# Kernel optimization log

Hardware: AMD Instinct MI355X
Metric: run time of the kernel (lower is better)

Reference implementation:

```python
import jax, jax.numpy as jnp
import numpy as np

# ROI Align config (module attributes in the original torch wrapper)
SPATIAL_SCALE = 0.25
POOLED_H = 7
POOLED_W = 7
SAMPLE_NUM = 2
ROI_END_MODE = 1  # Ascend: end coord gets +roi_end_mode before scaling


def setup_inputs() -> dict:
    key = jax.random.key(0)
    k_feat, k_b, k_xy, k_wh = jax.random.split(key, 4)
    B, C, H, W = 2, 256, 200, 200
    N = 1000
    feat = jax.random.normal(k_feat, (B, C, H, W), dtype=jnp.float32)
    img_h, img_w = H / SPATIAL_SCALE, W / SPATIAL_SCALE
    bidx = jax.random.randint(k_b, (N,), 0, B).astype(jnp.float32)
    xy = jax.random.uniform(k_xy, (N, 2), dtype=jnp.float32)
    wh = jax.random.uniform(k_wh, (N, 2), dtype=jnp.float32)
    x1 = xy[:, 0] * (img_w - 64.0)
    y1 = xy[:, 1] * (img_h - 64.0)
    x2 = x1 + 8.0 + wh[:, 0] * 200.0
    y2 = y1 + 8.0 + wh[:, 1] * 200.0
    rois = jnp.stack([bidx, x1, y1, x2, y2], axis=1)  # [N,5]
    return {"input": feat, "rois": rois}


def _axis_coords(start, bin_size, pooled, sn):
    # sample coord for grid index g: start + bin_size*(g+0.5)/sn, g in [0, pooled*sn)
    g = jnp.arange(pooled * sn, dtype=jnp.float32)
    return start[:, None] + bin_size[:, None] * (g[None, :] + 0.5) / sn  # [N, pooled*sn]


def _bilinear_1d(c, size):
    # returns (low_idx, high_idx, w_low, w_high, valid) for coordinate array c
    valid = (c >= -1.0) & (c <= size)
    cc = jnp.clip(c, 0.0, size - 1.0)
    lo = jnp.floor(cc).astype(jnp.int32)
    lo = jnp.clip(lo, 0, size - 1)
    hi = jnp.clip(lo + 1, 0, size - 1)
    frac = cc - lo.astype(jnp.float32)
    return lo, hi, 1.0 - frac, frac, valid


def roi_align(feat, rois):
    B, C, H, W = feat.shape
    N = rois.shape[0]
    bidx = rois[:, 0].astype(jnp.int32)
    off = float(ROI_END_MODE)
    x1 = rois[:, 1] * SPATIAL_SCALE
    y1 = rois[:, 2] * SPATIAL_SCALE
    x2 = (rois[:, 3] + off) * SPATIAL_SCALE
    y2 = (rois[:, 4] + off) * SPATIAL_SCALE
    roi_w = jnp.maximum(x2 - x1, 1.0)
    roi_h = jnp.maximum(y2 - y1, 1.0)
    bin_h = roi_h / POOLED_H
    bin_w = roi_w / POOLED_W

    ys = _axis_coords(y1, bin_h, POOLED_H, SAMPLE_NUM)  # [N, GY]
    xs = _axis_coords(x1, bin_w, POOLED_W, SAMPLE_NUM)  # [N, GX]
    yl, yh, wyl, wyh, vy = _bilinear_1d(ys, H)
    xl, xh, wxl, wxh, vx = _bilinear_1d(xs, W)

    b = bidx[:, None, None]

    def gather(yi, xi):
        # advanced indexing -> [N, GY, GX, C]
        return feat[b, :, yi[:, :, None], xi[:, None, :]]

    val = (wyl[:, :, None, None] * wxl[:, None, :, None] * gather(yl, xl)
           + wyl[:, :, None, None] * wxh[:, None, :, None] * gather(yl, xh)
           + wyh[:, :, None, None] * wxl[:, None, :, None] * gather(yh, xl)
           + wyh[:, :, None, None] * wxh[:, None, :, None] * gather(yh, xh))
    mask = (vy[:, :, None] & vx[:, None, :]).astype(val.dtype)[..., None]
    val = val * mask  # [N, GY, GX, C]

    # average pool over the SAMPLE_NUM x SAMPLE_NUM grid inside each bin
    val = val.reshape(N, POOLED_H, SAMPLE_NUM, POOLED_W, SAMPLE_NUM, C)
    out = val.mean(axis=(2, 4))  # [N, PH, PW, C]
    return jnp.transpose(out, (0, 3, 1, 2))  # [N, C, PH, PW]


def reference(input, rois):
    return roi_align(input, rois)
```

## Files before the change

### kernel.cpp

```cpp
#include <hip/hip_runtime.h>
#include <hip/hip_bf16.h>


constexpr int C_TOT  = 256;
constexpr int H_FEAT = 200;
constexpr int W_FEAT = 200;
constexpr int HW     = H_FEAT * W_FEAT;
constexpr int S_TOT  = 49;
constexpr size_t FEATT_BYTES = (size_t)2 * HW * C_TOT * sizeof(unsigned short);
constexpr int NXCD = 8;
constexpr int NBUCKET = 32;

__global__ __launch_bounds__(1024) void roi_bin_kernel(
    const float* __restrict__ rois, int* __restrict__ perm, int N)
{
    __shared__ int hist[NBUCKET];
    __shared__ int base[NBUCKET];
    __shared__ int cnt[NBUCKET];
    int t = threadIdx.x;

    if (t < NBUCKET) { hist[t] = 0; cnt[t] = 0; }
    __syncthreads();

    int bucket = -1;
    if (t < N) {
        const float* r = rois + (size_t)t * 5;
        int   b  = (int)r[0];
        float cx = (r[1] + r[3]) * 0.5f * 0.25f;
        float cy = (r[2] + r[4]) * 0.5f * 0.25f;
        int qx = min(max((int)(cx * (4.0f / 200.0f)), 0), 3);
        int qy = min(max((int)(cy * (4.0f / 200.0f)), 0), 3);
        bucket = ((b & 1) << 4) | (qy << 2) | qx;
        atomicAdd(&hist[bucket], 1);
    }
    __syncthreads();

    if (t == 0) {
        int acc = 0;
        for (int i = 0; i < NBUCKET; ++i) { base[i] = acc; acc += hist[i]; }
    }
    __syncthreads();

    if (t < N) {
        int pos = base[bucket] + atomicAdd(&cnt[bucket], 1);
        perm[pos] = t;
    }
}

__global__ __launch_bounds__(256) void nchw_to_nhwc_bf16_kernel(
    const float* __restrict__ feat,
    unsigned short* __restrict__ featT)
{
    __shared__ float tile[32][33];
    int tx = threadIdx.x;
    int ty = threadIdx.y;
    int s0 = blockIdx.x * 32;
    int c0 = blockIdx.y * 32;
    int b  = blockIdx.z;

    const float* src = feat + ((size_t)b * C_TOT) * HW;
    #pragma unroll
    for (int i = 0; i < 4; ++i) {
        int r = ty + i * 8;
        tile[r][tx] = src[(size_t)(c0 + r) * HW + (s0 + tx)];
    }
    __syncthreads();
    unsigned short* dst = featT + ((size_t)b * HW) * C_TOT;
    #pragma unroll
    for (int i = 0; i < 4; ++i) {
        int r = ty + i * 8;
        float x = tile[tx][r];
        unsigned int u = __float_as_uint(x);
        unsigned int rb = (u + 0x7fffu + ((u >> 16) & 1u)) >> 16;
        dst[(size_t)(s0 + r) * C_TOT + (c0 + tx)] = (unsigned short)rb;
    }
}

__global__ __launch_bounds__(512) void roi_align_nhwc_kernel(
    const unsigned short* __restrict__ featT,
    const float* __restrict__ rois,
    const int* __restrict__ perm,
    float* __restrict__ out,
    int N, int use_perm)
{
    __shared__ alignas(16) float tile[C_TOT * S_TOT];

    int n;
    if (use_perm) {
        int chunk = (N + NXCD - 1) / NXCD;
        int rank  = (blockIdx.x & (NXCD - 1)) * chunk + (blockIdx.x >> 3);
        if (rank >= N) rank = blockIdx.x;
        n = perm[rank];
    } else {
        n = blockIdx.x;
    }

    int tid  = threadIdx.x;
    int wave = tid >> 6;
    int lane = tid & 63;

    const float* r = rois + (size_t)n * 5;
    int   b  = (int)r[0];
    float x1 = r[1] * 0.25f;
    float y1 = r[2] * 0.25f;
    float x2 = (r[3] + 1.0f) * 0.25f;
    float y2 = (r[4] + 1.0f) * 0.25f;
    float bin_w = fmaxf(x2 - x1, 1.0f) * (1.0f / 7.0f);
    float bin_h = fmaxf(y2 - y1, 1.0f) * (1.0f / 7.0f);

    const unsigned short* fbase =
        featT + (size_t)b * HW * C_TOT + (size_t)lane * 4;

    for (int s = wave; s < S_TOT; s += 8) {
        int ph = s / 7;
        int pw = s - ph * 7;

        int   yoff[2][2];
        int   xoff[2][2];
        float wy[2][2], wx[2][2];
        #pragma unroll
        for (int i = 0; i < 2; ++i) {
            float gy  = (float)(2 * ph + i);
            float cy  = y1 + bin_h * ((gy + 0.5f) * 0.5f);
            bool  vy  = (cy >= -1.0f) && (cy <= (float)H_FEAT);
            float ccy = fminf(fmaxf(cy, 0.0f), (float)(H_FEAT - 1));
            int   ylo = (int)ccy;
            int   yhi = min(ylo + 1, H_FEAT - 1);
            float fy  = ccy - (float)ylo;
            yoff[i][0] = ylo * W_FEAT;
            yoff[i][1] = yhi * W_FEAT;
            wy[i][0] = vy ? (1.0f - fy) * 0.5f : 0.0f;
            wy[i][1] = vy ? fy * 0.5f          : 0.0f;

            float gx  = (float)(2 * pw + i);
            float cx  = x1 + bin_w * ((gx + 0.5f) * 0.5f);
            bool  vx  = (cx >= -1.0f) && (cx <= (float)W_FEAT);
            float ccx = fminf(fmaxf(cx, 0.0f), (float)(W_FEAT - 1));
            int   xlo = (int)ccx;
            int   xhi = min(xlo + 1, W_FEAT - 1);
            float fx  = ccx - (float)xlo;
            xoff[i][0] = xlo;
            xoff[i][1] = xhi;
            wx[i][0] = vx ? (1.0f - fx) * 0.5f : 0.0f;
            wx[i][1] = vx ? fx * 0.5f          : 0.0f;
        }

        float4 acc = make_float4(0.f, 0.f, 0.f, 0.f);
        #pragma unroll
        for (int iy = 0; iy < 2; ++iy)
        #pragma unroll
        for (int jy = 0; jy < 2; ++jy)
        #pragma unroll
        for (int ix = 0; ix < 2; ++ix)
        #pragma unroll
        for (int jx = 0; jx < 2; ++jx) {
            float w = wy[iy][jy] * wx[ix][jx];
            const ushort4 v = *reinterpret_cast<const ushort4*>(
                fbase + (size_t)(yoff[iy][jy] + xoff[ix][jx]) * C_TOT);
            float f0 = __uint_as_float((unsigned int)v.x << 16);
            float f1 = __uint_as_float((unsigned int)v.y << 16);
            float f2 = __uint_as_float((unsigned int)v.z << 16);
            float f3 = __uint_as_float((unsigned int)v.w << 16);
            acc.x = fmaf(w, f0, acc.x);
            acc.y = fmaf(w, f1, acc.y);
            acc.z = fmaf(w, f2, acc.z);
            acc.w = fmaf(w, f3, acc.w);
        }

        int c = lane * 4;
        tile[(c + 0) * S_TOT + s] = acc.x;
        tile[(c + 1) * S_TOT + s] = acc.y;
        tile[(c + 2) * S_TOT + s] = acc.z;
        tile[(c + 3) * S_TOT + s] = acc.w;
    }
    __syncthreads();

    const float4* t4 = reinterpret_cast<const float4*>(tile);
    float4* o4 = reinterpret_cast<float4*>(out + (size_t)n * (C_TOT * S_TOT));
    constexpr int Q = C_TOT * S_TOT / 4;
    for (int q = tid; q < Q; q += 512)
        o4[q] = t4[q];
}

constexpr int CPT = 4;
constexpr int CG  = C_TOT / CPT;

__global__ __launch_bounds__(256) void roi_align_direct_kernel(
    const float* __restrict__ feat,
    const float* __restrict__ rois,
    float* __restrict__ out,
    int N)
{
    int t = blockIdx.x * 256 + threadIdx.x;
    int total = N * CG * S_TOT;
    if (t >= total) return;

    int s   = t % S_TOT;
    int rem = t / S_TOT;
    int c0  = rem % CG;
    int n   = rem / CG;
    int ph  = s / 7;
    int pw  = s - ph * 7;

    const float* r = rois + (size_t)n * 5;
    int   b  = (int)r[0];
    float x1 = r[1] * 0.25f;
    float y1 = r[2] * 0.25f;
    float x2 = (r[3] + 1.0f) * 0.25f;
    float y2 = (r[4] + 1.0f) * 0.25f;
    float bin_w = fmaxf(x2 - x1, 1.0f) * (1.0f / 7.0f);
    float bin_h = fmaxf(y2 - y1, 1.0f) * (1.0f / 7.0f);

    int   roff[2][2], coff[2][2];
    float wy[2][2], wx[2][2];
    #pragma unroll
    for (int i = 0; i < 2; ++i) {
        float gy  = (float)(2 * ph + i);
        float cy  = y1 + bin_h * ((gy + 0.5f) * 0.5f);
        bool  vy  = (cy >= -1.0f) && (cy <= (float)H_FEAT);
        float ccy = fminf(fmaxf(cy, 0.0f), (float)(H_FEAT - 1));
        int   ylo = (int)ccy;
        int   yhi = min(ylo + 1, H_FEAT - 1);
        float fy  = ccy - (float)ylo;
        roff[i][0] = ylo * W_FEAT;
        roff[i][1] = yhi * W_FEAT;
        wy[i][0] = vy ? (1.0f - fy) : 0.0f;
        wy[i][1] = vy ? fy          : 0.0f;

        float gx  = (float)(2 * pw + i);
        float cx  = x1 + bin_w * ((gx + 0.5f) * 0.5f);
        bool  vx  = (cx >= -1.0f) && (cx <= (float)W_FEAT);
        float ccx = fminf(fmaxf(cx, 0.0f), (float)(W_FEAT - 1));
        int   xlo = (int)ccx;
        int   xhi = min(xlo + 1, W_FEAT - 1);
        float fx  = ccx - (float)xlo;
        coff[i][0] = xlo;
        coff[i][1] = xhi;
        wx[i][0] = vx ? (1.0f - fx) : 0.0f;
        wx[i][1] = vx ? fx          : 0.0f;
    }

    float w16[16];
    int   o16[16];
    #pragma unroll
    for (int iy = 0; iy < 2; ++iy)
    #pragma unroll
    for (int ix = 0; ix < 2; ++ix)
    #pragma unroll
    for (int jy = 0; jy < 2; ++jy)
    #pragma unroll
    for (int jx = 0; jx < 2; ++jx) {
        int idx = ((iy * 2 + ix) * 2 + jy) * 2 + jx;
        w16[idx] = wy[iy][jy] * wx[ix][jx];
        o16[idx] = roff[iy][jy] + coff[ix][jx];
    }

    size_t base  = ((size_t)b * C_TOT + c0) * HW;
    size_t obase = (size_t)n * (C_TOT * S_TOT) + (size_t)c0 * S_TOT + s;

    #pragma unroll
    for (int k = 0; k < CPT; ++k) {
        const float* f = feat + base + (size_t)k * CG * HW;
        float acc = 0.0f;
        #pragma unroll
        for (int j = 0; j < 16; ++j)
            acc = fmaf(w16[j], f[o16[j]], acc);
        out[obase + (size_t)k * (CG * S_TOT)] = acc * 0.25f;
    }
}

extern "C" void kernel_launch(void* const* d_in, const int* in_sizes, int n_in,
                              void* d_out, int out_size, void* d_ws, size_t ws_size,
                              hipStream_t stream) {
    const float* feat = (const float*)d_in[0];
    const float* rois = (const float*)d_in[1];
    float* out = (float*)d_out;
    int N = in_sizes[1] / 5;

    size_t need = FEATT_BYTES + 4096;
    if (ws_size >= need) {
        unsigned short* featT = (unsigned short*)d_ws;
        int* perm = (int*)((char*)d_ws + FEATT_BYTES);
        int use_perm = (N <= 1024) ? 1 : 0;
        if (use_perm)
            roi_bin_kernel<<<1, 1024, 0, stream>>>(rois, perm, N);
        dim3 tgrid(HW / 32, C_TOT / 32, 2);
        dim3 tblk(32, 8);
        nchw_to_nhwc_bf16_kernel<<<tgrid, tblk, 0, stream>>>(feat, featT);
        roi_align_nhwc_kernel<<<N, 512, 0, stream>>>(featT, rois, perm, out, N, use_perm);
    } else {
        int total  = N * CG * S_TOT;
        int blocks = (total + 255) / 256;
        roi_align_direct_kernel<<<blocks, 256, 0, stream>>>(feat, rois, out, N);
    }
}
```

Measured before the change: 61.12 us.

## Use 16-byte bf16 loads split across half-waves with XOR-swizzled LDS tile

Each half-wave now handles one of the two horizontal neighbor pixels, and each lane loads 8 bf16 channels with one 16-byte load instead of 4 channels with 8-byte loads. The two halves are summed with a cross-lane shuffle. The shared tile uses an XOR swizzle on channel index to spread LDS bank conflicts, and the output copy undoes the swizzle. This halves the number of global load instructions but adds shuffles, per-element index math in the copy-out, and idle lanes during tile writes.

```diff
diff --git a/kernel.cpp b/kernel.cpp
--- a/kernel.cpp
+++ b/kernel.cpp
@@ -98,6 +98,8 @@
     int tid  = threadIdx.x;
     int wave = tid >> 6;
     int lane = tid & 63;
+    int half = lane >> 5;
+    int li   = lane & 31;
 
     const float* r = rois + (size_t)n * 5;
     int   b  = (int)r[0];
@@ -108,8 +110,8 @@
     float bin_w = fmaxf(x2 - x1, 1.0f) * (1.0f / 7.0f);
     float bin_h = fmaxf(y2 - y1, 1.0f) * (1.0f / 7.0f);
 
-    const unsigned short* fbase =
-        featT + (size_t)b * HW * C_TOT + (size_t)lane * 4;
+    const unsigned short* fb = featT + (size_t)b * HW * C_TOT + li * 8;
+    int xorsw = (li >> 2) & 7;
 
     for (int s = wave; s < S_TOT; s += 8) {
         int ph = s / 7;
@@ -145,41 +147,66 @@
             wx[i][1] = vx ? fx * 0.5f          : 0.0f;
         }
 
-        float4 acc = make_float4(0.f, 0.f, 0.f, 0.f);
+        float acc[8];
+        #pragma unroll
+        for (int j = 0; j < 8; ++j) acc[j] = 0.0f;
+
         #pragma unroll
         for (int iy = 0; iy < 2; ++iy)
         #pragma unroll
         for (int jy = 0; jy < 2; ++jy)
         #pragma unroll
-        for (int ix = 0; ix < 2; ++ix)
-        #pragma unroll
-        for (int jx = 0; jx < 2; ++jx) {
-            float w = wy[iy][jy] * wx[ix][jx];
-            const ushort4 v = *reinterpret_cast<const ushort4*>(
-                fbase + (size_t)(yoff[iy][jy] + xoff[ix][jx]) * C_TOT);
-            float f0 = __uint_as_float((unsigned int)v.x << 16);
-            float f1 = __uint_as_float((unsigned int)v.y << 16);
-            float f2 = __uint_as_float((unsigned int)v.z << 16);
-            float f3 = __uint_as_float((unsigned int)v.w << 16);
-            acc.x = fmaf(w, f0, acc.x);
-            acc.y = fmaf(w, f1, acc.y);
-            acc.z = fmaf(w, f2, acc.z);
-            acc.w = fmaf(w, f3, acc.w);
+        for (int ix = 0; ix < 2; ++ix) {
+            int   pixA = yoff[iy][jy] + xoff[ix][0];
+            int   pixB = yoff[iy][jy] + xoff[ix][1];
+            float wA   = wy[iy][jy] * wx[ix][0];
+            float wB   = wy[iy][jy] * wx[ix][1];
+            int   pix  = half ? pixB : pixA;
+            float w    = half ? wB   : wA;
+            const uint4 v = *reinterpret_cast<const uint4*>(
+                fb + (size_t)pix * C_TOT);
+            unsigned int u;
+            u = v.x;
+            acc[0] = fmaf(w, __uint_as_float(u << 16),          acc[0]);
+            acc[1] = fmaf(w, __uint_as_float(u & 0xffff0000u),  acc[1]);
+            u = v.y;
+            acc[2] = fmaf(w, __uint_as_float(u << 16),          acc[2]);
+            acc[3] = fmaf(w, __uint_as_float(u & 0xffff0000u),  acc[3]);
+            u = v.z;
+            acc[4] = fmaf(w, __uint_as_float(u << 16),          acc[4]);
+            acc[5] = fmaf(w, __uint_as_float(u & 0xffff0000u),  acc[5]);
+            u = v.w;
+            acc[6] = fmaf(w, __uint_as_float(u << 16),          acc[6]);
+            acc[7] = fmaf(w, __uint_as_float(u & 0xffff0000u),  acc[7]);
         }
 
-        int c = lane * 4;
-        tile[(c + 0) * S_TOT + s] = acc.x;
-        tile[(c + 1) * S_TOT + s] = acc.y;
-        tile[(c + 2) * S_TOT + s] = acc.z;
-        tile[(c + 3) * S_TOT + s] = acc.w;
-    }
-    __syncthreads();
-
-    const float4* t4 = reinterpret_cast<const float4*>(tile);
+        #pragma unroll
+        for (int j = 0; j < 8; ++j) {
+            float sum = acc[j] + __shfl_xor(acc[j], 32);
+            if (half == 0) {
+                int slot_ch = li * 8 + (j ^ xorsw);
+                tile[slot_ch * S_TOT + s] = sum;
+            }
+        }
+    }
+    __syncthreads();
+
     float4* o4 = reinterpret_cast<float4*>(out + (size_t)n * (C_TOT * S_TOT));
-    constexpr int Q = C_TOT * S_TOT / 4;
-    for (int q = tid; q < Q; q += 512)
-        o4[q] = t4[q];
+    constexpr int Q4 = C_TOT * S_TOT / 4;
+    for (int q4 = tid; q4 < Q4; q4 += 512) {
+        int q = q4 * 4;
+        float4 val;
+        float* vp = reinterpret_cast<float*>(&val);
+        #pragma unroll
+        for (int e = 0; e < 4; ++e) {
+            int qq = q + e;
+            int ch = qq / S_TOT;
+            int ss = qq - ch * S_TOT;
+            int slot_ch = (ch & ~7) | ((ch & 7) ^ ((ch >> 5) & 7));
+            vp[e] = tile[slot_ch * S_TOT + ss];
+        }
+        o4[q4] = val;
+    }
 }
 
 constexpr int CPT = 4;
```

Result: no change. 61.16 us, median of 2 (+0.1%).
